# Kernel optimization log

Measured on AMD Instinct MI355X. Metric: run time of the kernel, lower is better.

The kernel has to match this reference:

```python
import jax, jax.numpy as jnp
import numpy as np

C = 1.0
TEMPERATURE = 1.0
EPS = 1e-10
N, D = 8192, 512


def setup_inputs() -> dict:
    key = jax.random.key(0)
    k1, k2 = jax.random.split(key)
    # scale so embeddings lie inside the unit (Poincare) ball: norms ~0.5
    scale = 0.5 / np.sqrt(D)
    audio = jax.random.normal(k1, (N, D), dtype=jnp.float32) * scale
    text = jax.random.normal(k2, (N, D), dtype=jnp.float32) * scale
    labels = jnp.arange(N, dtype=jnp.int32)
    return {"audio_features": audio, "text_features": text, "labels": labels}


def _hyperbolic_similarity(a, b):
    # pairwise squared distance via norm expansion (avoids N x N x D tensor)
    a2 = jnp.sum(a * a, axis=-1)            # [N]
    b2 = jnp.sum(b * b, axis=-1)            # [M]
    diff_sq = a2[:, None] + b2[None, :] - 2.0 * (a @ b.T)  # [N, M]
    a2c = jnp.minimum(a2, 1.0 - EPS)
    b2c = jnp.minimum(b2, 1.0 - EPS)
    denom = jnp.maximum((1.0 - a2c)[:, None] * (1.0 - b2c)[None, :], EPS)
    arg = jnp.maximum(1.0 + 2.0 * diff_sq / denom, 1.0 + EPS)
    dist = jnp.arccosh(arg) / jnp.sqrt(jnp.asarray(C, a.dtype))
    return -dist / TEMPERATURE


def _cross_entropy(logits, labels):
    logp = jax.nn.log_softmax(logits, axis=-1)
    picked = jnp.take_along_axis(logp, labels[:, None], axis=-1)[:, 0]
    return -jnp.mean(picked)


def reference(audio_features, text_features, labels):
    sim = _hyperbolic_similarity(audio_features, text_features)  # [N, M]
    loss_audio = _cross_entropy(sim, labels)
    loss_text = _cross_entropy(sim.T, labels)
    return (loss_audio + loss_text) * 0.5
```

## Files before the change

### kernel.cpp

```cpp
#include <hip/hip_runtime.h>
#include <hip/hip_bf16.h>


#define NROWS 8192
#define DDIM  512
#define BM 128
#define BN 128
#define BK 128
#define NT (DDIM / BK)
#define LDSBUF 32768

typedef __attribute__((ext_vector_type(4))) float f32x4;

constexpr float EPSF = 1e-10f;
constexpr float DOT_SCALE = 1.0f / 1024.0f;

#define GLOAD_LDS16(g, l)                                                        \
    __builtin_amdgcn_global_load_lds(                                            \
        (const __attribute__((address_space(1))) void*)(g),                      \
        (__attribute__((address_space(3))) void*)(l), 16, 0, 0)

__device__ inline unsigned int f2e4m3(float f) {
    union { float f; unsigned int u; } x; x.f = f;
    unsigned int s = (x.u >> 24) & 0x80u;
    float af = __builtin_fabsf(f);
    unsigned int r;
    if (af >= 0.015625f) {
        unsigned int m = x.u & 0x7fffffffu;
        m += 0x000fffffu + ((m >> 20) & 1u);
        r = ((m >> 20) - (120u << 3)) & 0x7fu;
    } else {
        int q = (int)rintf(af * 512.0f);
        r = (unsigned int)q;
    }
    return r | s;
}

__global__ __launch_bounds__(256) void convert_norms(const float* __restrict__ audio,
                                                     const float* __restrict__ text,
                                                     unsigned char* __restrict__ Aq,
                                                     unsigned char* __restrict__ Bq,
                                                     float* __restrict__ a2,
                                                     float* __restrict__ b2,
                                                     float* __restrict__ diag,
                                                     float* __restrict__ zbuf) {
    if (blockIdx.x < 32) {
        int z = blockIdx.x * 512 + threadIdx.x * 2;
        *(float2*)(zbuf + z) = make_float2(0.f, 0.f);
    }
    int wave = threadIdx.x >> 6;
    int lane = threadIdx.x & 63;
    int row  = blockIdx.x * 4 + wave;
    const float* ra = audio + (size_t)row * DDIM + lane * 8;
    const float* rt = text  + (size_t)row * DDIM + lane * 8;
    float4 a0 = *(const float4*)(ra), a1 = *(const float4*)(ra + 4);
    float4 t0 = *(const float4*)(rt), t1 = *(const float4*)(rt + 4);

    float sa = a0.x*a0.x + a0.y*a0.y + a0.z*a0.z + a0.w*a0.w
             + a1.x*a1.x + a1.y*a1.y + a1.z*a1.z + a1.w*a1.w;
    float st = t0.x*t0.x + t0.y*t0.y + t0.z*t0.z + t0.w*t0.w
             + t1.x*t1.x + t1.y*t1.y + t1.z*t1.z + t1.w*t1.w;
    float dt = a0.x*t0.x + a0.y*t0.y + a0.z*t0.z + a0.w*t0.w
             + a1.x*t1.x + a1.y*t1.y + a1.z*t1.z + a1.w*t1.w;

    uint2 pa, pt;
    pa.x = f2e4m3(a0.x*32.f) | (f2e4m3(a0.y*32.f) << 8) |
           (f2e4m3(a0.z*32.f) << 16) | (f2e4m3(a0.w*32.f) << 24);
    pa.y = f2e4m3(a1.x*32.f) | (f2e4m3(a1.y*32.f) << 8) |
           (f2e4m3(a1.z*32.f) << 16) | (f2e4m3(a1.w*32.f) << 24);
    pt.x = f2e4m3(t0.x*32.f) | (f2e4m3(t0.y*32.f) << 8) |
           (f2e4m3(t0.z*32.f) << 16) | (f2e4m3(t0.w*32.f) << 24);
    pt.y = f2e4m3(t1.x*32.f) | (f2e4m3(t1.y*32.f) << 8) |
           (f2e4m3(t1.z*32.f) << 16) | (f2e4m3(t1.w*32.f) << 24);
    *(uint2*)(Aq + (size_t)row * DDIM + lane * 8) = pa;
    *(uint2*)(Bq + (size_t)row * DDIM + lane * 8) = pt;

    #pragma unroll
    for (int m = 1; m < 64; m <<= 1) {
        sa += __shfl_xor(sa, m);
        st += __shfl_xor(st, m);
        dt += __shfl_xor(dt, m);
    }
    if (lane == 0) {
        a2[row] = sa;
        b2[row] = st;
        float a2c  = fminf(sa, 1.0f - EPSF);
        float b2c  = fminf(st, 1.0f - EPSF);
        float diff = sa + st - 2.0f * dt;
        float den  = fmaxf((1.0f - a2c) * (1.0f - b2c), EPSF);
        float arg  = fmaxf(1.0f + 2.0f * diff / den, 1.0f + EPSF);
        diag[row]  = -logf(arg + sqrtf(arg * arg - 1.0f));
    }
}

__global__ __launch_bounds__(512, 4) void hyper_gemm(
    const unsigned char* __restrict__ A, const unsigned char* __restrict__ B,
    const float* __restrict__ a2, const float* __restrict__ b2,
    float* __restrict__ rowsum, float* __restrict__ colsum) {

    __shared__ char lds[2 * LDSBUF];

    const int tid  = threadIdx.x;
    const int lane = tid & 63;
    const int w    = tid >> 6;
    const int wm   = w >> 2;
    const int wn   = w & 3;

    const int bid = blockIdx.x;
    const int idx = bid >> 3;
    const int by  = (bid & 7) * 8 + (idx & 7);
    const int bx  = idx >> 3;
    const int i0 = by * BM;
    const int j0 = bx * BN;

    const int g  = lane >> 4;
    const int cl = lane & 15;

    const int srow = lane >> 3;
    const int scol = (((lane & 7) ^ srow)) * 16;
    const unsigned char* aP[2]; const unsigned char* bP[2]; int ldsOff[2];
    #pragma unroll
    for (int c = 0; c < 2; ++c) {
        int row = w * 16 + c * 8 + srow;
        aP[c] = A + (size_t)(i0 + row) * DDIM + scol;
        bP[c] = B + (size_t)(j0 + row) * DDIM + scol;
        ldsOff[c] = w * 2048 + c * 1024;
    }

    int addrA[4][4], addrB[2][4];
    #pragma unroll
    for (int mi = 0; mi < 4; ++mi) {
        int row = wm * 64 + mi * 16 + cl;
        int s = (row & 7) << 4;
        #pragma unroll
        for (int ks = 0; ks < 4; ++ks)
            addrA[mi][ks] = row * 128 + ((ks * 32 + g * 8) ^ s);
    }
    #pragma unroll
    for (int ni = 0; ni < 2; ++ni) {
        int row = wn * 32 + ni * 16 + cl;
        int s = (row & 7) << 4;
        #pragma unroll
        for (int ks = 0; ks < 4; ++ks)
            addrB[ni][ks] = 16384 + row * 128 + ((ks * 32 + g * 8) ^ s);
    }

    f32x4 acc[4][2];
    #pragma unroll
    for (int mi = 0; mi < 4; ++mi)
        #pragma unroll
        for (int ni = 0; ni < 2; ++ni)
            acc[mi][ni] = (f32x4)0.0f;

#define STAGE(buf, t)                                                     \
    do {                                                                  \
        _Pragma("unroll")                                                 \
        for (int c = 0; c < 2; ++c) {                                     \
            GLOAD_LDS16(aP[c] + (t) * BK,                                 \
                        lds + (buf) * LDSBUF + ldsOff[c]);                \
            GLOAD_LDS16(bP[c] + (t) * BK,                                 \
                        lds + (buf) * LDSBUF + 16384 + ldsOff[c]);        \
        }                                                                 \
    } while (0)

#define COMPUTE(buf)                                                      \
    do {                                                                  \
        _Pragma("unroll")                                                 \
        for (int ks = 0; ks < 4; ++ks) {                                  \
            long av[4]; long bv[2];                                       \
            _Pragma("unroll")                                             \
            for (int mi = 0; mi < 4; ++mi)                                \
                av[mi] = *(const long*)(lds + (buf) * LDSBUF + addrA[mi][ks]); \
            _Pragma("unroll")                                             \
            for (int ni = 0; ni < 2; ++ni)                                \
                bv[ni] = *(const long*)(lds + (buf) * LDSBUF + addrB[ni][ks]); \
            _Pragma("unroll")                                             \
            for (int mi = 0; mi < 4; ++mi)                                \
                _Pragma("unroll")                                         \
                for (int ni = 0; ni < 2; ++ni)                            \
                    acc[mi][ni] = __builtin_amdgcn_mfma_f32_16x16x32_fp8_fp8( \
                        av[mi], bv[ni], acc[mi][ni], 0, 0, 0);            \
        }                                                                 \
    } while (0)

    STAGE(0, 0);
    __syncthreads();
    #pragma unroll
    for (int t = 0; t < NT; ++t) {
        if (t + 1 < NT) STAGE((t + 1) & 1, t + 1);
        COMPUTE(t & 1);
        if (t + 1 < NT) __syncthreads();
    }
#undef STAGE
#undef COMPUTE

    float B2c[2], fb[2];
    #pragma unroll
    for (int ni = 0; ni < 2; ++ni) {
        float B2 = b2[j0 + wn * 32 + ni * 16 + cl];
        B2c[ni] = B2;
        fb[ni] = __builtin_amdgcn_rcpf(1.0f - fminf(B2, 1.0f - EPSF));
    }

    float cp[2] = {0.f, 0.f};
    #pragma unroll
    for (int mi = 0; mi < 4; ++mi) {
        #pragma unroll
        for (int reg = 0; reg < 4; ++reg) {
            int   gi  = i0 + wm * 64 + mi * 16 + g * 4 + reg;
            float A2  = a2[gi];
            float fa  = 2.0f * __builtin_amdgcn_rcpf(1.0f - fminf(A2, 1.0f - EPSF));
            float rsum = 0.f;
            #pragma unroll
            for (int ni = 0; ni < 2; ++ni) {
                float dot  = acc[mi][ni][reg];
                float diff = fmaf(-2.0f * DOT_SCALE, dot, A2 + B2c[ni]);
                float arg  = fmaf(diff * fa, fb[ni], 1.0f);
                arg = fmaxf(arg, 1.0f);
                float sq = sqrtf(fmaf(arg, arg, -1.0f));
                float e  = arg - sq;
                rsum += e;
                cp[ni] += e;
            }
            float v = rsum;
            v += __shfl_xor(v, 1); v += __shfl_xor(v, 2);
            v += __shfl_xor(v, 4); v += __shfl_xor(v, 8);
            if (cl == 0) atomicAdd(&rowsum[gi], v);
        }
    }
    #pragma unroll
    for (int ni = 0; ni < 2; ++ni) {
        float v = cp[ni];
        v += __shfl_xor(v, 16); v += __shfl_xor(v, 32);
        if (g == 0) atomicAdd(&colsum[j0 + wn * 32 + ni * 16 + cl], v);
    }
}

__global__ __launch_bounds__(1024) void finalize(const float* __restrict__ rowsum,
                                                 const float* __restrict__ colsum,
                                                 const float* __restrict__ diag,
                                                 float* __restrict__ out) {
    float s = 0.f;
    for (int i = threadIdx.x; i < NROWS; i += 1024)
        s += logf(rowsum[i]) + logf(colsum[i]) - 2.0f * diag[i];
    __shared__ float red[16];
    int lane = threadIdx.x & 63, wv = threadIdx.x >> 6;
    #pragma unroll
    for (int m = 1; m < 64; m <<= 1) s += __shfl_xor(s, m);
    if (lane == 0) red[wv] = s;
    __syncthreads();
    if (threadIdx.x == 0) {
        float t = 0.f;
        #pragma unroll
        for (int k = 0; k < 16; ++k) t += red[k];
        out[0] = t / (2.0f * NROWS);
    }
}

extern "C" void kernel_launch(void* const* d_in, const int* in_sizes, int n_in,
                              void* d_out, int out_size, void* d_ws, size_t ws_size,
                              hipStream_t stream) {
    const float* audio = (const float*)d_in[0];
    const float* text  = (const float*)d_in[1];
    float* out = (float*)d_out;

    char* ws = (char*)d_ws;
    const size_t BF = (size_t)NROWS * DDIM;
    unsigned char* Aq = (unsigned char*)ws;
    unsigned char* Bq = (unsigned char*)(ws + BF);
    float* a2     = (float*)(ws + 2 * BF);
    float* b2     = a2 + NROWS;
    float* rowsum = b2 + NROWS;
    float* colsum = rowsum + NROWS;
    float* diag   = colsum + NROWS;

    convert_norms<<<NROWS / 4, 256, 0, stream>>>(audio, text, Aq, Bq, a2, b2, diag, rowsum);
    hyper_gemm<<<(NROWS / BM) * (NROWS / BN), 512, 0, stream>>>(Aq, Bq, a2, b2, rowsum, colsum);
    finalize<<<1, 1024, 0, stream>>>(rowsum, colsum, diag, out);
}
```

Baseline: 212.6 us.

## Use 16x16x128 scaled FP8 MFMA with permuted quantized layout

Switches the FP8 GEMM inner loop from the 16x16x32 FP8 MFMA to the gfx950 scaled 16x16x128 f8f6f4 MFMA, which has neutral scales (127) and does four times the K per instruction. The quantization prepass now writes the FP8 operands in a permuted K order. This lets each lane fetch its 32 contiguous bytes with two 16-byte LDS reads instead of four 8-byte reads. The aim is fewer MFMA issues and fewer LDS instructions. The fallback path is adjusted to the new layout, and correctness relies on the K permutation matching the same way for both A and B.

```diff
diff --git a/kernel.cpp b/kernel.cpp
--- a/kernel.cpp
+++ b/kernel.cpp
@@ -11,6 +11,8 @@
 #define LDSBUF 32768
 
 typedef __attribute__((ext_vector_type(4))) float f32x4;
+typedef __attribute__((ext_vector_type(4))) int   i32x4;
+typedef __attribute__((ext_vector_type(8))) int   i32x8;
 
 constexpr float EPSF = 1e-10f;
 constexpr float DOT_SCALE = 1.0f / 1024.0f;
@@ -72,8 +74,15 @@
            (f2e4m3(t0.z*32.f) << 16) | (f2e4m3(t0.w*32.f) << 24);
     pt.y = f2e4m3(t1.x*32.f) | (f2e4m3(t1.y*32.f) << 8) |
            (f2e4m3(t1.z*32.f) << 16) | (f2e4m3(t1.w*32.f) << 24);
-    *(uint2*)(Aq + (size_t)row * DDIM + lane * 8) = pa;
-    *(uint2*)(Bq + (size_t)row * DDIM + lane * 8) = pt;
+
+    {
+        int c  = lane >> 4;
+        int gq = lane & 3;
+        int ks = (lane >> 2) & 3;
+        size_t opos = (size_t)row * DDIM + c * 128 + gq * 32 + ks * 8;
+        *(uint2*)(Aq + opos) = pa;
+        *(uint2*)(Bq + opos) = pt;
+    }
 
     #pragma unroll
     for (int m = 1; m < 64; m <<= 1) {
@@ -127,22 +136,22 @@
         ldsOff[c] = w * 2048 + c * 1024;
     }
 
-    int addrA[4][4], addrB[2][4];
+    int addrA[4][2], addrB[2][2];
     #pragma unroll
     for (int mi = 0; mi < 4; ++mi) {
         int row = wm * 64 + mi * 16 + cl;
         int s = (row & 7) << 4;
         #pragma unroll
-        for (int ks = 0; ks < 4; ++ks)
-            addrA[mi][ks] = row * 128 + ((ks * 32 + g * 8) ^ s);
+        for (int h = 0; h < 2; ++h)
+            addrA[mi][h] = row * 128 + ((g * 32 + h * 16) ^ s);
     }
     #pragma unroll
     for (int ni = 0; ni < 2; ++ni) {
         int row = wn * 32 + ni * 16 + cl;
         int s = (row & 7) << 4;
         #pragma unroll
-        for (int ks = 0; ks < 4; ++ks)
-            addrB[ni][ks] = 16384 + row * 128 + ((ks * 32 + g * 8) ^ s);
+        for (int h = 0; h < 2; ++h)
+            addrB[ni][h] = 16384 + row * 128 + ((g * 32 + h * 16) ^ s);
     }
 
     f32x4 acc[4][2];
@@ -163,6 +172,32 @@
         }                                                                 \
     } while (0)
 
+#if __has_builtin(__builtin_amdgcn_mfma_scale_f32_16x16x128_f8f6f4)
+#define COMPUTE(buf)                                                      \
+    do {                                                                  \
+        i32x8 av[4], bv[2];                                               \
+        _Pragma("unroll")                                                 \
+        for (int mi = 0; mi < 4; ++mi) {                                  \
+            i32x4 lo = *(const i32x4*)(lds + (buf) * LDSBUF + addrA[mi][0]); \
+            i32x4 hi = *(const i32x4*)(lds + (buf) * LDSBUF + addrA[mi][1]); \
+            av[mi][0]=lo[0]; av[mi][1]=lo[1]; av[mi][2]=lo[2]; av[mi][3]=lo[3]; \
+            av[mi][4]=hi[0]; av[mi][5]=hi[1]; av[mi][6]=hi[2]; av[mi][7]=hi[3]; \
+        }                                                                 \
+        _Pragma("unroll")                                                 \
+        for (int ni = 0; ni < 2; ++ni) {                                  \
+            i32x4 lo = *(const i32x4*)(lds + (buf) * LDSBUF + addrB[ni][0]); \
+            i32x4 hi = *(const i32x4*)(lds + (buf) * LDSBUF + addrB[ni][1]); \
+            bv[ni][0]=lo[0]; bv[ni][1]=lo[1]; bv[ni][2]=lo[2]; bv[ni][3]=lo[3]; \
+            bv[ni][4]=hi[0]; bv[ni][5]=hi[1]; bv[ni][6]=hi[2]; bv[ni][7]=hi[3]; \
+        }                                                                 \
+        _Pragma("unroll")                                                 \
+        for (int mi = 0; mi < 4; ++mi)                                    \
+            _Pragma("unroll")                                             \
+            for (int ni = 0; ni < 2; ++ni)                                \
+                acc[mi][ni] = __builtin_amdgcn_mfma_scale_f32_16x16x128_f8f6f4( \
+                    av[mi], bv[ni], acc[mi][ni], 0, 0, 0, 127, 0, 127);   \
+    } while (0)
+#else
 #define COMPUTE(buf)                                                      \
     do {                                                                  \
         _Pragma("unroll")                                                 \
@@ -170,10 +205,12 @@
             long av[4]; long bv[2];                                       \
             _Pragma("unroll")                                             \
             for (int mi = 0; mi < 4; ++mi)                                \
-                av[mi] = *(const long*)(lds + (buf) * LDSBUF + addrA[mi][ks]); \
+                av[mi] = *(const long*)(lds + (buf) * LDSBUF              \
+                          + addrA[mi][ks >> 1] + (ks & 1) * 8);           \
             _Pragma("unroll")                                             \
             for (int ni = 0; ni < 2; ++ni)                                \
-                bv[ni] = *(const long*)(lds + (buf) * LDSBUF + addrB[ni][ks]); \
+                bv[ni] = *(const long*)(lds + (buf) * LDSBUF              \
+                          + addrB[ni][ks >> 1] + (ks & 1) * 8);           \
             _Pragma("unroll")                                             \
             for (int mi = 0; mi < 4; ++mi)                                \
                 _Pragma("unroll")                                         \
@@ -182,6 +219,7 @@
                         av[mi], bv[ni], acc[mi][ni], 0, 0, 0);            \
         }                                                                 \
     } while (0)
+#endif
 
     STAGE(0, 0);
     __syncthreads();
```

Measured after the change: 418.0 us. +96.6%, slower.

## Permute FP8 operand layout so MFMA fragments load as 16-byte LDS reads

Applied to the files above, without the earlier changes.

The quantization kernel now writes FP8 values in a permuted order within each 128-byte K-chunk, so each lane's two k-steps sit next to each other. The GEMM then issues one 128-bit LDS read per fragment instead of two 64-bit reads, halving the LDS load instruction count and the address registers. The permutation has to match exactly between the prepass writes and the swizzled LDS reads, and it changes how the XOR swizzle interacts with bank access patterns.

```diff
diff --git a/kernel.cpp b/kernel.cpp
--- a/kernel.cpp
+++ b/kernel.cpp
@@ -11,6 +11,7 @@
 #define LDSBUF 32768
 
 typedef __attribute__((ext_vector_type(4))) float f32x4;
+typedef __attribute__((ext_vector_type(2))) long  i64x2;
 
 constexpr float EPSF = 1e-10f;
 constexpr float DOT_SCALE = 1.0f / 1024.0f;
@@ -72,8 +73,15 @@
            (f2e4m3(t0.z*32.f) << 16) | (f2e4m3(t0.w*32.f) << 24);
     pt.y = f2e4m3(t1.x*32.f) | (f2e4m3(t1.y*32.f) << 8) |
            (f2e4m3(t1.z*32.f) << 16) | (f2e4m3(t1.w*32.f) << 24);
-    *(uint2*)(Aq + (size_t)row * DDIM + lane * 8) = pa;
-    *(uint2*)(Bq + (size_t)row * DDIM + lane * 8) = pt;
+
+    {
+        int c  = lane >> 4;
+        int gq = lane & 3;
+        int ks = (lane >> 2) & 3;
+        size_t opos = (size_t)row * DDIM + c * 128 + gq * 32 + ks * 8;
+        *(uint2*)(Aq + opos) = pa;
+        *(uint2*)(Bq + opos) = pt;
+    }
 
     #pragma unroll
     for (int m = 1; m < 64; m <<= 1) {
@@ -127,22 +135,22 @@
         ldsOff[c] = w * 2048 + c * 1024;
     }
 
-    int addrA[4][4], addrB[2][4];
+    int addrA[4][2], addrB[2][2];
     #pragma unroll
     for (int mi = 0; mi < 4; ++mi) {
         int row = wm * 64 + mi * 16 + cl;
         int s = (row & 7) << 4;
         #pragma unroll
-        for (int ks = 0; ks < 4; ++ks)
-            addrA[mi][ks] = row * 128 + ((ks * 32 + g * 8) ^ s);
+        for (int h = 0; h < 2; ++h)
+            addrA[mi][h] = row * 128 + ((g * 32 + h * 16) ^ s);
     }
     #pragma unroll
     for (int ni = 0; ni < 2; ++ni) {
         int row = wn * 32 + ni * 16 + cl;
         int s = (row & 7) << 4;
         #pragma unroll
-        for (int ks = 0; ks < 4; ++ks)
-            addrB[ni][ks] = 16384 + row * 128 + ((ks * 32 + g * 8) ^ s);
+        for (int h = 0; h < 2; ++h)
+            addrB[ni][h] = 16384 + row * 128 + ((g * 32 + h * 16) ^ s);
     }
 
     f32x4 acc[4][2];
@@ -166,20 +174,22 @@
 #define COMPUTE(buf)                                                      \
     do {                                                                  \
         _Pragma("unroll")                                                 \
-        for (int ks = 0; ks < 4; ++ks) {                                  \
-            long av[4]; long bv[2];                                       \
+        for (int h = 0; h < 2; ++h) {                                     \
+            i64x2 va[4], vb[2];                                           \
             _Pragma("unroll")                                             \
             for (int mi = 0; mi < 4; ++mi)                                \
-                av[mi] = *(const long*)(lds + (buf) * LDSBUF + addrA[mi][ks]); \
+                va[mi] = *(const i64x2*)(lds + (buf) * LDSBUF + addrA[mi][h]); \
             _Pragma("unroll")                                             \
             for (int ni = 0; ni < 2; ++ni)                                \
-                bv[ni] = *(const long*)(lds + (buf) * LDSBUF + addrB[ni][ks]); \
+                vb[ni] = *(const i64x2*)(lds + (buf) * LDSBUF + addrB[ni][h]); \
             _Pragma("unroll")                                             \
-            for (int mi = 0; mi < 4; ++mi)                                \
+            for (int half = 0; half < 2; ++half)                          \
                 _Pragma("unroll")                                         \
-                for (int ni = 0; ni < 2; ++ni)                            \
-                    acc[mi][ni] = __builtin_amdgcn_mfma_f32_16x16x32_fp8_fp8( \
-                        av[mi], bv[ni], acc[mi][ni], 0, 0, 0);            \
+                for (int mi = 0; mi < 4; ++mi)                            \
+                    _Pragma("unroll")                                     \
+                    for (int ni = 0; ni < 2; ++ni)                        \
+                        acc[mi][ni] = __builtin_amdgcn_mfma_f32_16x16x32_fp8_fp8( \
+                            va[mi][half], vb[ni][half], acc[mi][ni], 0, 0, 0);    \
         }                                                                 \
     } while (0)
 
```

Result: faster. 203.0 us (-4.5%).
